# Performance work log

Hardware: AMD Instinct MI355X
Metric: run time of the kernel (lower is better)

Reference implementation:

```python
import jax, jax.numpy as jnp
import numpy as np

B, T, H, C = 64, 512, 1024, 21  # batch, seq_len, hidden_size, num_labels


def setup_inputs() -> dict:
    key = jax.random.key(0)
    ks = jax.random.split(key, 7)
    hidden_states = jax.random.normal(ks[0], (B, T, H), dtype=jnp.float32)
    lengths = jax.random.randint(ks[1], (B,), 1, T + 1)  # at least 1 valid token
    attention_mask = jnp.arange(T)[None, :] < lengths[:, None]  # [B,T] bool, contiguous prefix
    labels = jax.random.randint(ks[2], (B, T), 0, C)
    # classifier params (nn.Linear(H, C))
    W = jax.random.normal(ks[3], (H, C), dtype=jnp.float32) * 0.02
    b = jnp.zeros((C,), dtype=jnp.float32)
    # CRF params (torchcrf init: uniform(-0.1, 0.1))
    transitions = jax.random.uniform(ks[4], (C, C), minval=-0.1, maxval=0.1, dtype=jnp.float32)
    start_transitions = jax.random.uniform(ks[5], (C,), minval=-0.1, maxval=0.1, dtype=jnp.float32)
    end_transitions = jax.random.uniform(ks[6], (C,), minval=-0.1, maxval=0.1, dtype=jnp.float32)
    return {
        "hidden_states": hidden_states,
        "W": W,
        "b": b,
        "transitions": transitions,
        "start_transitions": start_transitions,
        "end_transitions": end_transitions,
        "attention_mask": attention_mask,
        "labels": labels,
    }


def _crf_nll(emissions, tags, mask, transitions, start_transitions, end_transitions):
    """Mean negative log-likelihood of torchcrf CRF(batch_first=True, reduction='mean')."""
    maskf = mask.astype(emissions.dtype)
    # ---- numerator: score of the gold tag path ----
    em_tag = jnp.take_along_axis(emissions, tags[..., None], axis=2)[..., 0]  # [B,T]
    trans_score = transitions[tags[:, :-1], tags[:, 1:]]                      # [B,T-1]
    num = (start_transitions[tags[:, 0]] + em_tag[:, 0]
           + jnp.sum((trans_score + em_tag[:, 1:]) * maskf[:, 1:], axis=1))
    last_idx = jnp.sum(mask.astype(jnp.int32), axis=1) - 1                    # [B]
    last_tag = jnp.take_along_axis(tags, last_idx[:, None], axis=1)[:, 0]
    num = num + end_transitions[last_tag]
    # ---- denominator: forward algorithm (log partition) ----
    alpha0 = start_transitions[None, :] + emissions[:, 0]                     # [B,C]

    def step(alpha, xs):
        em_t, m_t = xs  # [B,C], [B]
        nxt = jax.nn.logsumexp(alpha[:, :, None] + transitions[None, :, :] + em_t[:, None, :], axis=1)
        return jnp.where(m_t[:, None], nxt, alpha), None

    xs = (jnp.swapaxes(emissions[:, 1:], 0, 1), jnp.swapaxes(mask[:, 1:], 0, 1))
    alphaT, _ = jax.lax.scan(step, alpha0, xs)
    logZ = jax.nn.logsumexp(alphaT + end_transitions[None, :], axis=1)        # [B]
    llh = num - logZ
    return -jnp.mean(llh)


def reference(hidden_states, W, b, transitions, start_transitions, end_transitions,
              attention_mask, labels):
    # dropout is identity at inference; emissions = Linear(hidden)
    emissions = jnp.einsum('bth,hc->btc', hidden_states, W) + b              # [B,T,C]
    # mask logic from the module: attention_mask & (labels != -100); mask[:,0] = True
    mask = attention_mask & (labels != -100)
    mask = mask.at[:, 0].set(True)
    loss = _crf_nll(emissions, labels, mask, transitions, start_transitions, end_transitions)
    return emissions, loss
```

## Files before the change

### kernel.cpp

```cpp
#include <hip/hip_runtime.h>

#define BB 64
#define TT 512
#define HH 1024
#define CC 21
#define NROWS (BB*TT)

__global__ __launch_bounds__(512) void emis_gemm(const float* __restrict__ hs,
                                                 const float* __restrict__ W,
                                                 const float* __restrict__ bias,
                                                 float* __restrict__ out) {
  __shared__ float lds[17728];
  const int tid  = threadIdx.x;
  const int lane = tid & 63;
  const int w    = __builtin_amdgcn_readfirstlane(tid >> 6);
  const int row0 = blockIdx.x * 64;

  if (blockIdx.x == 0 && tid == 0) out[(size_t)NROWS * CC] = 0.f;

  float acc[CC];
#pragma unroll
  for (int c = 0; c < CC; ++c) acc[c] = 0.f;

  const int r_  = (tid) >> 4,        c4_  = tid & 15;
  const int r2_ = (tid + 512) >> 4;

  float4 buf0, buf1;
  buf0 = *reinterpret_cast<const float4*>(hs + (size_t)(row0 + r_ ) * HH + c4_ * 4);
  buf1 = *reinterpret_cast<const float4*>(hs + (size_t)(row0 + r2_) * HH + c4_ * 4);
  {
    float* t0 = &lds[r_  * 65 + c4_ * 4];
    float* t1 = &lds[r2_ * 65 + c4_ * 4];
    t0[0] = buf0.x; t0[1] = buf0.y; t0[2] = buf0.z; t0[3] = buf0.w;
    t1[0] = buf1.x; t1[1] = buf1.y; t1[2] = buf1.z; t1[3] = buf1.w;
  }
  __syncthreads();

  for (int chunk = 0; chunk < 16; ++chunk) {
    const int cur = (chunk & 1) * 4160;
    const int nxt = ((chunk + 1) & 1) * 4160;
    if (chunk < 15) {
      const int k0n = (chunk + 1) * 64;
      buf0 = *reinterpret_cast<const float4*>(hs + (size_t)(row0 + r_ ) * HH + k0n + c4_ * 4);
      buf1 = *reinterpret_cast<const float4*>(hs + (size_t)(row0 + r2_) * HH + k0n + c4_ * 4);
    }
    const float* Wp = W + (size_t)(chunk * 64 + w * 8) * CC;
#pragma unroll
    for (int kk = 0; kk < 8; ++kk) {
      float x = lds[cur + lane * 65 + w * 8 + kk];
#pragma unroll
      for (int c = 0; c < CC; ++c) acc[c] = fmaf(x, Wp[kk * CC + c], acc[c]);
    }
    if (chunk < 15) {
      float* t0 = &lds[nxt + r_  * 65 + c4_ * 4];
      float* t1 = &lds[nxt + r2_ * 65 + c4_ * 4];
      t0[0] = buf0.x; t0[1] = buf0.y; t0[2] = buf0.z; t0[3] = buf0.w;
      t1[0] = buf1.x; t1[1] = buf1.y; t1[2] = buf1.z; t1[3] = buf1.w;
    }
    __syncthreads();
  }

  if (w > 0) {
#pragma unroll
    for (int c = 0; c < CC; ++c)
      lds[8320 + (w - 1) * 1344 + lane * CC + c] = acc[c];
  }
  __syncthreads();
  if (w == 0) {
#pragma unroll
    for (int c = 0; c < CC; ++c) {
      float v = acc[c] + bias[c];
#pragma unroll
      for (int q = 0; q < 7; ++q) v += lds[8320 + q * 1344 + lane * CC + c];
      lds[lane * CC + c] = v;
    }
  }
  __syncthreads();
  for (int idx = tid; idx < 1344; idx += 512)
    out[(size_t)row0 * CC + idx] = lds[idx];
}

__global__ __launch_bounds__(128) void crf_kernel(const float* __restrict__ em,
                                                  const float* __restrict__ trans,
                                                  const float* __restrict__ startT,
                                                  const float* __restrict__ endT,
                                                  const int* __restrict__ att,
                                                  const int* __restrict__ labels,
                                                  float* __restrict__ loss) {
  const int b    = blockIdx.x;
  const int tid  = threadIdx.x;
  const int wave = tid >> 6;
  const int lane = tid & 63;
  __shared__ float sh_num;
  __shared__ int   sh_len;

  const float L2E = 1.4426950408889634f;
  const float LN2 = 0.6931471805599453f;

  if (wave == 1) {
    int cnt = 0;
    for (int t = lane; t < TT; t += 64) {
      bool m = (t == 0) || ((att[b * TT + t] != 0) && (labels[b * TT + t] != -100));
      cnt += m ? 1 : 0;
    }
#pragma unroll
    for (int off = 32; off >= 1; off >>= 1) cnt += __shfl_down(cnt, off);
    cnt = __shfl(cnt, 0);

    float s = 0.f;
    for (int t = lane + 1; t < TT; t += 64) {
      bool m = (att[b * TT + t] != 0) && (labels[b * TT + t] != -100);
      if (m) {
        int tp = labels[b * TT + t - 1], tc = labels[b * TT + t];
        s += trans[tp * CC + tc] + em[((size_t)b * TT + t) * CC + tc];
      }
    }
#pragma unroll
    for (int off = 32; off >= 1; off >>= 1) s += __shfl_down(s, off);
    if (lane == 0) {
      int tag0 = labels[b * TT];
      int lastTag = labels[b * TT + cnt - 1];
      s += startT[tag0] + em[((size_t)b * TT) * CC + tag0] + endT[lastTag];
      sh_num = s;
      sh_len = cnt;
    }
  }

  const int j = lane < CC ? lane : CC - 1;
  float E[CC];
  float beta = 0.f, endE = 0.f;
  if (wave == 0) {
#pragma unroll
    for (int i = 0; i < CC; ++i)
      E[i] = __builtin_amdgcn_exp2f(trans[i * CC + j] * L2E);
    beta = __builtin_amdgcn_exp2f((startT[j] + em[((size_t)b * TT) * CC + j]) * L2E);
    endE = __builtin_amdgcn_exp2f(endT[j] * L2E);
  }
  __syncthreads();

  if (wave == 0) {
    const int len = sh_len;
    int ksum = 0;

    float sb[CC];
#pragma unroll
    for (int i = 0; i < CC; ++i)
      sb[i] = __int_as_float(__builtin_amdgcn_readlane(__float_as_int(beta), i));

    const float* emB = em + (size_t)b * TT * CC;

    auto step = [&](float em_v) {
      float pm = __builtin_amdgcn_exp2f(em_v * L2E);
      int ef = (__float_as_int(sb[0]) >> 23) & 255;
      ksum += ef - 127;
      float pms = pm * __int_as_float((254 - ef) << 23);
      float c0 = 0.f, c1 = 0.f, c2 = 0.f;
#pragma unroll
      for (int i = 0; i < CC; i += 3) c0 = fmaf(sb[i], E[i], c0);
#pragma unroll
      for (int i = 1; i < CC; i += 3) c1 = fmaf(sb[i], E[i], c1);
#pragma unroll
      for (int i = 2; i < CC; i += 3) c2 = fmaf(sb[i], E[i], c2);
      beta = ((c0 + c1) + c2) * pms;
#pragma unroll
      for (int i = 0; i < CC; ++i)
        sb[i] = __int_as_float(__builtin_amdgcn_readlane(__float_as_int(beta), i));
    };

    float r[8];
#pragma unroll
    for (int u = 0; u < 8; ++u) {
      int tt = 1 + u; if (tt > len - 1) tt = len - 1;
      r[u] = emB[(size_t)tt * CC + j];
    }

    int t = 1;
    for (; t + 8 <= len; t += 8) {
#pragma unroll
      for (int u = 0; u < 8; ++u) {
        int tp = t + u + 8; if (tp > len - 1) tp = len - 1;
        float rn = emB[(size_t)tp * CC + j];
        step(r[u]);
        r[u] = rn;
      }
    }
    for (; t < len; ++t) {
      step(r[0]);
#pragma unroll
      for (int u = 0; u < 7; ++u) r[u] = r[u + 1];
    }

    float v = (lane < CC) ? beta * endE : 0.f;
#pragma unroll
    for (int off = 32; off >= 1; off >>= 1) v += __shfl_xor(v, off);
    if (lane == 0) {
      float logZ = (float)ksum * LN2 + LN2 * __builtin_amdgcn_logf(v);
      atomicAdd(loss, -(sh_num - logZ) * (1.0f / 64.0f));
    }
  }
}

extern "C" void kernel_launch(void* const* d_in, const int* in_sizes, int n_in,
                              void* d_out, int out_size, void* d_ws, size_t ws_size,
                              hipStream_t stream) {
  const float* hs     = (const float*)d_in[0];
  const float* W      = (const float*)d_in[1];
  const float* bias   = (const float*)d_in[2];
  const float* trans  = (const float*)d_in[3];
  const float* startT = (const float*)d_in[4];
  const float* endT   = (const float*)d_in[5];
  const int*   att    = (const int*)d_in[6];
  const int*   labels = (const int*)d_in[7];
  float* out = (float*)d_out;

  emis_gemm<<<dim3(512), dim3(512), 0, stream>>>(hs, W, bias, out);
  crf_kernel<<<dim3(64), dim3(128), 0, stream>>>(out, trans, startT, endT, att,
                                                 labels, out + (size_t)NROWS * CC);
}
```

Baseline: 296.7 us.

## Register-resident GEMM without LDS staging and bidirectional CRF forward-backward recursion

The emission GEMM drops LDS staging and double-buffered syncs. Each thread now streams its own row segment of hidden states directly into registers, and W rows are prefetched into register double buffers. Each block covers 128 rows split into four K segments, which are reduced through LDS. The CRF partition function now runs forward and backward recursions at the same time from both ends, meeting in the middle, which halves the serial dependency chain length at the cost of more registers and a backward pass with different scaling.

```diff
diff --git a/kernel.cpp b/kernel.cpp
--- a/kernel.cpp
+++ b/kernel.cpp
@@ -6,78 +6,88 @@
 #define CC 21
 #define NROWS (BB*TT)
 
-__global__ __launch_bounds__(512) void emis_gemm(const float* __restrict__ hs,
-                                                 const float* __restrict__ W,
-                                                 const float* __restrict__ bias,
-                                                 float* __restrict__ out) {
-  __shared__ float lds[17728];
+__global__ __launch_bounds__(512, 2) void emis_gemm(const float* __restrict__ hs,
+                                                    const float* __restrict__ W,
+                                                    const float* __restrict__ bias,
+                                                    float* __restrict__ out) {
+  __shared__ float red[4 * 128 * CC];
   const int tid  = threadIdx.x;
   const int lane = tid & 63;
   const int w    = __builtin_amdgcn_readfirstlane(tid >> 6);
-  const int row0 = blockIdx.x * 64;
+  const int half = w >> 2;
+  const int seg  = w & 3;
+  const int rowL = half * 64 + lane;
+  const int row0 = blockIdx.x * 128;
 
   if (blockIdx.x == 0 && tid == 0) out[(size_t)NROWS * CC] = 0.f;
 
+  const float4* xrow =
+      reinterpret_cast<const float4*>(hs + (size_t)(row0 + rowL) * HH + seg * 256);
+  const float4* Wf4 = reinterpret_cast<const float4*>(W);
+  const int nw0 = seg * 64;
+
+  float4 xq[8];
+#pragma unroll
+  for (int i = 0; i < 8; ++i) xq[i] = xrow[i];
+
+  float4 wb[2][21];
+  {
+    const float4* p = Wf4 + (size_t)nw0 * 21;
+#pragma unroll
+    for (int q = 0; q < 21; ++q) wb[0][q] = p[q];
+  }
+
   float acc[CC];
 #pragma unroll
   for (int c = 0; c < CC; ++c) acc[c] = 0.f;
 
-  const int r_  = (tid) >> 4,        c4_  = tid & 15;
-  const int r2_ = (tid + 512) >> 4;
-
-  float4 buf0, buf1;
-  buf0 = *reinterpret_cast<const float4*>(hs + (size_t)(row0 + r_ ) * HH + c4_ * 4);
-  buf1 = *reinterpret_cast<const float4*>(hs + (size_t)(row0 + r2_) * HH + c4_ * 4);
-  {
-    float* t0 = &lds[r_  * 65 + c4_ * 4];
-    float* t1 = &lds[r2_ * 65 + c4_ * 4];
-    t0[0] = buf0.x; t0[1] = buf0.y; t0[2] = buf0.z; t0[3] = buf0.w;
-    t1[0] = buf1.x; t1[1] = buf1.y; t1[2] = buf1.z; t1[3] = buf1.w;
+#pragma unroll 8
+  for (int kb = 0; kb < 64; ++kb) {
+    const int s = kb & 7;
+    float4 xv = xq[s];
+    int kn = kb + 8; if (kn > 63) kn = 63;
+    xq[s] = xrow[kn];
+    int nw = nw0 + kb + 1; if (nw > 255) nw = 255;
+    {
+      const float4* p = Wf4 + (size_t)nw * 21;
+      float4* dst = wb[(kb + 1) & 1];
+#pragma unroll
+      for (int q = 0; q < 21; ++q) dst[q] = p[q];
+    }
+    const float4* wc = wb[kb & 1];
+#pragma unroll
+    for (int r = 0; r < 4; ++r) {
+      float xr = (r == 0) ? xv.x : (r == 1) ? xv.y : (r == 2) ? xv.z : xv.w;
+#pragma unroll
+      for (int c = 0; c < CC; ++c) {
+        const int f = r * 21 + c;
+        const int q = f >> 2, m = f & 3;
+        float4 ww = wc[q];
+        float wv = (m == 0) ? ww.x : (m == 1) ? ww.y : (m == 2) ? ww.z : ww.w;
+        acc[c] = fmaf(xr, wv, acc[c]);
+      }
+    }
+  }
+
+  if (seg != 0) {
+#pragma unroll
+    for (int c = 0; c < CC; ++c)
+      red[((seg - 1) * 128 + rowL) * CC + c] = acc[c];
   }
   __syncthreads();
-
-  for (int chunk = 0; chunk < 16; ++chunk) {
-    const int cur = (chunk & 1) * 4160;
-    const int nxt = ((chunk + 1) & 1) * 4160;
-    if (chunk < 15) {
-      const int k0n = (chunk + 1) * 64;
-      buf0 = *reinterpret_cast<const float4*>(hs + (size_t)(row0 + r_ ) * HH + k0n + c4_ * 4);
-      buf1 = *reinterpret_cast<const float4*>(hs + (size_t)(row0 + r2_) * HH + k0n + c4_ * 4);
-    }
-    const float* Wp = W + (size_t)(chunk * 64 + w * 8) * CC;
-#pragma unroll
-    for (int kk = 0; kk < 8; ++kk) {
-      float x = lds[cur + lane * 65 + w * 8 + kk];
-#pragma unroll
-      for (int c = 0; c < CC; ++c) acc[c] = fmaf(x, Wp[kk * CC + c], acc[c]);
-    }
-    if (chunk < 15) {
-      float* t0 = &lds[nxt + r_  * 65 + c4_ * 4];
-      float* t1 = &lds[nxt + r2_ * 65 + c4_ * 4];
-      t0[0] = buf0.x; t0[1] = buf0.y; t0[2] = buf0.z; t0[3] = buf0.w;
-      t1[0] = buf1.x; t1[1] = buf1.y; t1[2] = buf1.z; t1[3] = buf1.w;
-    }
-    __syncthreads();
-  }
-
-  if (w > 0) {
-#pragma unroll
-    for (int c = 0; c < CC; ++c)
-      lds[8320 + (w - 1) * 1344 + lane * CC + c] = acc[c];
-  }
-  __syncthreads();
-  if (w == 0) {
+  if (seg == 0) {
 #pragma unroll
     for (int c = 0; c < CC; ++c) {
       float v = acc[c] + bias[c];
 #pragma unroll
-      for (int q = 0; q < 7; ++q) v += lds[8320 + q * 1344 + lane * CC + c];
-      lds[lane * CC + c] = v;
+      for (int q = 0; q < 3; ++q) v += red[(q * 128 + rowL) * CC + c];
+      red[(3 * 128 + rowL) * CC + c] = v;
     }
   }
   __syncthreads();
-  for (int idx = tid; idx < 1344; idx += 512)
-    out[(size_t)row0 * CC + idx] = lds[idx];
+  const float* fin = red + 3 * 128 * CC;
+  for (int idx = tid; idx < 128 * CC; idx += 512)
+    out[(size_t)row0 * CC + idx] = fin[idx];
 }
 
 __global__ __launch_bounds__(128) void crf_kernel(const float* __restrict__ em,
@@ -127,76 +137,97 @@
   }
 
   const int j = lane < CC ? lane : CC - 1;
-  float E[CC];
-  float beta = 0.f, endE = 0.f;
+  float E[CC], F[CC];
+  float f = 0.f, g = 0.f;
   if (wave == 0) {
 #pragma unroll
-    for (int i = 0; i < CC; ++i)
+    for (int i = 0; i < CC; ++i) {
       E[i] = __builtin_amdgcn_exp2f(trans[i * CC + j] * L2E);
-    beta = __builtin_amdgcn_exp2f((startT[j] + em[((size_t)b * TT) * CC + j]) * L2E);
-    endE = __builtin_amdgcn_exp2f(endT[j] * L2E);
+      F[i] = __builtin_amdgcn_exp2f(trans[j * CC + i] * L2E);
+    }
+    f = __builtin_amdgcn_exp2f((startT[j] + em[((size_t)b * TT) * CC + j]) * L2E);
+    g = __builtin_amdgcn_exp2f(endT[j] * L2E);
   }
   __syncthreads();
-
-  if (wave == 0) {
-    const int len = sh_len;
-    int ksum = 0;
-
-    float sb[CC];
-#pragma unroll
-    for (int i = 0; i < CC; ++i)
-      sb[i] = __int_as_float(__builtin_amdgcn_readlane(__float_as_int(beta), i));
-
-    const float* emB = em + (size_t)b * TT * CC;
-
-    auto step = [&](float em_v) {
-      float pm = __builtin_amdgcn_exp2f(em_v * L2E);
-      int ef = (__float_as_int(sb[0]) >> 23) & 255;
-      ksum += ef - 127;
-      float pms = pm * __int_as_float((254 - ef) << 23);
-      float c0 = 0.f, c1 = 0.f, c2 = 0.f;
-#pragma unroll
-      for (int i = 0; i < CC; i += 3) c0 = fmaf(sb[i], E[i], c0);
-#pragma unroll
-      for (int i = 1; i < CC; i += 3) c1 = fmaf(sb[i], E[i], c1);
-#pragma unroll
-      for (int i = 2; i < CC; i += 3) c2 = fmaf(sb[i], E[i], c2);
-      beta = ((c0 + c1) + c2) * pms;
-#pragma unroll
-      for (int i = 0; i < CC; ++i)
-        sb[i] = __int_as_float(__builtin_amdgcn_readlane(__float_as_int(beta), i));
-    };
-
-    float r[8];
-#pragma unroll
-    for (int u = 0; u < 8; ++u) {
-      int tt = 1 + u; if (tt > len - 1) tt = len - 1;
-      r[u] = emB[(size_t)tt * CC + j];
-    }
-
-    int t = 1;
-    for (; t + 8 <= len; t += 8) {
-#pragma unroll
-      for (int u = 0; u < 8; ++u) {
-        int tp = t + u + 8; if (tp > len - 1) tp = len - 1;
-        float rn = emB[(size_t)tp * CC + j];
-        step(r[u]);
-        r[u] = rn;
-      }
-    }
-    for (; t < len; ++t) {
-      step(r[0]);
-#pragma unroll
-      for (int u = 0; u < 7; ++u) r[u] = r[u + 1];
-    }
-
-    float v = (lane < CC) ? beta * endE : 0.f;
-#pragma unroll
-    for (int off = 32; off >= 1; off >>= 1) v += __shfl_xor(v, off);
-    if (lane == 0) {
-      float logZ = (float)ksum * LN2 + LN2 * __builtin_amdgcn_logf(v);
-      atomicAdd(loss, -(sh_num - logZ) * (1.0f / 64.0f));
-    }
+  if (wave != 0) return;
+
+  const int len = sh_len;
+  const int L  = len - 1;
+  const int mF = (L + 1) >> 1;
+  const int mB = L - mF;
+  int kf = 0, kg = 0;
+
+  float sf[CC];
+#pragma unroll
+  for (int i = 0; i < CC; ++i)
+    sf[i] = __int_as_float(__builtin_amdgcn_readlane(__float_as_int(f), i));
+
+  const float* emB = em + (size_t)b * TT * CC;
+
+  float rf[4], rb[4];
+#pragma unroll
+  for (int u = 0; u < 4; ++u) {
+    int tf = 1 + u; if (tf > TT - 1) tf = TT - 1;
+    rf[u] = emB[(size_t)tf * CC + j];
+    int tb = len - 1 - u; if (tb < 0) tb = 0;
+    rb[u] = emB[(size_t)tb * CC + j];
+  }
+
+  int it = 0;
+  while (it < mF) {
+#pragma unroll
+    for (int u = 0; u < 4; ++u) {
+      const int i2 = it + u;
+      if (i2 < mF) {
+        float pm = __builtin_amdgcn_exp2f(rf[u] * L2E);
+        int tp = 1 + i2 + 4; if (tp > TT - 1) tp = TT - 1;
+        rf[u] = emB[(size_t)tp * CC + j];
+        int ef = (__float_as_int(sf[0]) >> 23) & 255;
+        kf += ef - 127;
+        float pms = pm * __int_as_float((254 - ef) << 23);
+        float c0 = 0.f, c1 = 0.f, c2 = 0.f;
+#pragma unroll
+        for (int i = 0; i < CC; i += 3) c0 = fmaf(sf[i], E[i], c0);
+#pragma unroll
+        for (int i = 1; i < CC; i += 3) c1 = fmaf(sf[i], E[i], c1);
+#pragma unroll
+        for (int i = 2; i < CC; i += 3) c2 = fmaf(sf[i], E[i], c2);
+        f = ((c0 + c1) + c2) * pms;
+#pragma unroll
+        for (int i = 0; i < CC; ++i)
+          sf[i] = __int_as_float(__builtin_amdgcn_readlane(__float_as_int(f), i));
+      }
+      if (i2 < mB) {
+        float pm = __builtin_amdgcn_exp2f(rb[u] * L2E);
+        int tb = len - 1 - i2 - 4; if (tb < 0) tb = 0;
+        rb[u] = emB[(size_t)tb * CC + j];
+        float h = pm * g;
+        float sh_[CC];
+#pragma unroll
+        for (int i = 0; i < CC; ++i)
+          sh_[i] = __int_as_float(__builtin_amdgcn_readlane(__float_as_int(h), i));
+        int eg = (__float_as_int(sh_[0]) >> 23) & 255;
+        kg += eg - 127;
+        float sB = __int_as_float((254 - eg) << 23);
+        float d0 = 0.f, d1 = 0.f, d2 = 0.f;
+#pragma unroll
+        for (int i = 0; i < CC; i += 3) d0 = fmaf(sh_[i], F[i], d0);
+#pragma unroll
+        for (int i = 1; i < CC; i += 3) d1 = fmaf(sh_[i], F[i], d1);
+#pragma unroll
+        for (int i = 2; i < CC; i += 3) d2 = fmaf(sh_[i], F[i], d2);
+        g = ((d0 + d1) + d2) * sB;
+      }
+    }
+    it += 4;
+  }
+
+  float v = (lane < CC) ? f * g : 0.f;
+#pragma unroll
+  for (int off = 32; off >= 1; off >>= 1) v += __shfl_xor(v, off);
+  if (lane == 0) {
+    float logZ = (float)(kf + kg) * LN2 + LN2 * __builtin_amdgcn_logf(v);
+    atomicAdd(loss, -(sh_num - logZ) * (1.0f / 64.0f));
   }
 }
 
@@ -213,7 +244,7 @@
   const int*   labels = (const int*)d_in[7];
   float* out = (float*)d_out;
 
-  emis_gemm<<<dim3(512), dim3(512), 0, stream>>>(hs, W, bias, out);
+  emis_gemm<<<dim3(256), dim3(512), 0, stream>>>(hs, W, bias, out);
   crf_kernel<<<dim3(64), dim3(128), 0, stream>>>(out, trans, startT, endT, att,
                                                  labels, out + (size_t)NROWS * CC);
 }
```

New measurement: 326.7 us. 10.1% more time.
